# Kernel optimization log

Hardware: AMD Instinct MI355X
Metric: run time of the kernel (lower is better)

The kernel has to match this reference:

```python
import jax, jax.numpy as jnp
import numpy as np

B, S, H, K = 16, 1024, 1024, 256


def _span(x, Ws, bs, start, end):
    # x: [B,S,H]; start/end: [B,K] int indices into the S axis
    def proj(W, b):
        return jnp.einsum('bsh,oh->bso', x, W) + b  # nn.Linear: x @ W.T + b

    def gather(p, idx):
        # batched index_select along seq axis -> [B,K,H]
        return jnp.take_along_axis(p, idx[..., None], axis=1)

    p1, p2, p3, p4 = (proj(W, b) for W, b in zip(Ws, bs))
    span = (gather(p1, start) + gather(p2, end)
            + (gather(p3, start) - gather(p3, end))
            + gather(p4, start) * gather(p4, end))
    return jnp.tanh(span)


def setup_inputs() -> dict:
    key = jax.random.key(0)
    ks = jax.random.split(key, 20)
    inp = {
        'hidden_states': jax.random.normal(ks[0], (B, S, H), dtype=jnp.float32),
        'prem_word_idxs': jax.random.randint(ks[1], (B, 1, 2, K), 0, S, dtype=jnp.int64) if jax.config.read('jax_enable_x64') else jax.random.randint(ks[1], (B, 1, 2, K), 0, S).astype(jnp.int32),
        'hypo_word_idxs': jax.random.randint(ks[2], (B, 1, 2, K), 0, S).astype(jnp.int32),
    }
    names = ['Wp1', 'bp1', 'Wp2', 'bp2', 'Wp3', 'bp3', 'Wp4', 'bp4',
             'Wh1', 'bh1', 'Wh2', 'bh2', 'Wh3', 'bh3', 'Wh4', 'bh4']
    for i, n in enumerate(names):
        k = ks[3 + i]
        if n.startswith('W'):
            inp[n] = jax.random.normal(k, (H, H), dtype=jnp.float32) * 0.02
        else:
            inp[n] = jax.random.normal(k, (H,), dtype=jnp.float32) * 0.02
    return inp


def reference(hidden_states, prem_word_idxs, hypo_word_idxs,
              Wp1, bp1, Wp2, bp2, Wp3, bp3, Wp4, bp4,
              Wh1, bh1, Wh2, bh2, Wh3, bh3, Wh4, bh4):
    p_idx = prem_word_idxs[:, 0]  # squeeze(1) -> [B,2,K]
    h_idx = hypo_word_idxs[:, 0]
    prem_h_ij = _span(hidden_states, (Wp1, Wp2, Wp3, Wp4), (bp1, bp2, bp3, bp4),
                      p_idx[:, 0], p_idx[:, 1])
    hypo_h_ij = _span(hidden_states, (Wh1, Wh2, Wh3, Wh4), (bh1, bh2, bh3, bh4),
                      h_idx[:, 0], h_idx[:, 1])
    return (prem_h_ij, hypo_h_ij)
```

## Files before the change

kernel.cpp:

```cpp
#include <hip/hip_runtime.h>
#include <hip/hip_bf16.h>

typedef _Float16 f16;
typedef _Float16 f16x4 __attribute__((ext_vector_type(4)));
typedef _Float16 f16x8 __attribute__((ext_vector_type(8)));
typedef float    f32x4 __attribute__((ext_vector_type(4)));

#define H_DIM 1024
#define S_DIM 1024
#define PLANE (1024*1024)
#define MT 128
#define NT 64
#define KT 32
#define XOFF (6*PLANE)

__device__ __forceinline__ void load_lds16(const f16* g, f16* l) {
    __builtin_amdgcn_global_load_lds(
        (const __attribute__((address_space(1))) void*)g,
        (__attribute__((address_space(3))) void*)l, 16, 0, 0);
}

__global__ __launch_bounds__(256) void prep_weights(
    const float* __restrict__ Wp1, const float* __restrict__ Wp2,
    const float* __restrict__ Wp3, const float* __restrict__ Wp4,
    const float* __restrict__ Wh1, const float* __restrict__ Wh2,
    const float* __restrict__ Wh3, const float* __restrict__ Wh4,
    f16* __restrict__ ws)
{
    const int span = blockIdx.y;
    const float* W1 = span ? Wh1 : Wp1;
    const float* W2 = span ? Wh2 : Wp2;
    const float* W3 = span ? Wh3 : Wp3;
    const float* W4 = span ? Wh4 : Wp4;
    f16* base = ws + (size_t)span * 3 * PLANE;

    size_t i = ((size_t)blockIdx.x * 256 + threadIdx.x) * 4;
    f32x4 w1 = *(const f32x4*)(W1 + i);
    f32x4 w2 = *(const f32x4*)(W2 + i);
    f32x4 w3 = *(const f32x4*)(W3 + i);
    f32x4 w4 = *(const f32x4*)(W4 + i);

    f16x4 wa, wb, wc;
#pragma unroll
    for (int j = 0; j < 4; ++j) {
        wa[j] = (f16)(w1[j] + w3[j]);
        wb[j] = (f16)(w2[j] - w3[j]);
        wc[j] = (f16)w4[j];
    }
    *(f16x4*)(base + 0*PLANE + i) = wa;
    *(f16x4*)(base + 1*PLANE + i) = wb;
    *(f16x4*)(base + 2*PLANE + i) = wc;
}

__global__ __launch_bounds__(256) void prep_x(const float* __restrict__ x,
                                              f16* __restrict__ xh)
{
    size_t i = ((size_t)blockIdx.x * 256 + threadIdx.x) * 4;
    f32x4 v = *(const f32x4*)(x + i);
    f16x4 h;
#pragma unroll
    for (int j = 0; j < 4; ++j) h[j] = (f16)v[j];
    *(f16x4*)(xh + i) = h;
}

__global__ __launch_bounds__(256) void span_gemm(
    const f16* __restrict__ xh,
    const int* __restrict__ idxP, const int* __restrict__ idxH,
    const f16* __restrict__ wpl,
    const float* __restrict__ bp1, const float* __restrict__ bp2, const float* __restrict__ bp4,
    const float* __restrict__ bh1, const float* __restrict__ bh2, const float* __restrict__ bh4,
    float* __restrict__ out)
{
    const int t     = threadIdx.x;
    const int mtile = blockIdx.x;
    const int ntile = blockIdx.y;
    const int span  = blockIdx.z;

    const int* idx   = span ? idxH : idxP;
    const f16* wbase = wpl + (size_t)span * 3 * PLANE;
    const float* b1 = span ? bh1 : bp1;
    const float* b2 = span ? bh2 : bp2;
    const float* b4 = span ? bh4 : bp4;
    float* obase = out + (size_t)span * 4096 * H_DIM;

    __shared__ __align__(16) f16 A_lds[2][2 * MT * KT];
    __shared__ __align__(16) f16 B_lds[2][3 * NT * KT];
    __shared__ int rowoff[2][MT];

    {
        int side = t >> 7;
        int m = t & 127;
        int bk = mtile * MT + m;
        int b  = bk >> 8;
        int kk = bk & 255;
        int id = idx[b * 512 + side * 256 + kk];
        rowoff[side][m] = (b * S_DIM + id) * H_DIM;
    }
    __syncthreads();

    const int wid  = t >> 6;
    const int lane = t & 63;

    const f16* asrc[4]; int adst[4];
#pragma unroll
    for (int j = 0; j < 4; ++j) {
        int o = wid * 4 + j;
        int p = o >> 3, g = o & 7;
        int r = g * 16 + (lane >> 2);
        asrc[j] = xh + rowoff[p][r] + (lane & 3) * 8;
        adst[j] = p * (MT * KT) + g * 16 * KT;
    }
    const f16* bsrc[3]; int bdst[3];
#pragma unroll
    for (int j = 0; j < 3; ++j) {
        int o = wid * 3 + j;
        int p = o >> 2, g = o & 3;
        int grow = ntile * NT + g * 16 + (lane >> 2);
        bsrc[j] = wbase + (size_t)p * PLANE + (size_t)grow * H_DIM + (lane & 3) * 8;
        bdst[j] = p * (NT * KT) + g * 16 * KT;
    }

    f32x4 accL[4][2], accP[4][2], accQ[4][2];
    {
        f32x4 z = {0.f, 0.f, 0.f, 0.f};
#pragma unroll
        for (int mf = 0; mf < 4; ++mf)
#pragma unroll
            for (int nf = 0; nf < 2; ++nf) { accL[mf][nf] = z; accP[mf][nf] = z; accQ[mf][nf] = z; }
    }

    const int wm   = (wid & 1) * 64;
    const int wn   = (wid >> 1) * 32;
    const int lrow = lane & 15;
    const int lq   = lane >> 4;

#pragma unroll
    for (int j = 0; j < 4; ++j) load_lds16(asrc[j], &A_lds[0][adst[j]]);
#pragma unroll
    for (int j = 0; j < 3; ++j) load_lds16(bsrc[j], &B_lds[0][bdst[j]]);
    __syncthreads();

    for (int ks = 0; ks < H_DIM / KT; ++ks) {
        const int cur = ks & 1;
        if (ks < H_DIM / KT - 1) {
            const int k0 = (ks + 1) * KT;
            const int nb = cur ^ 1;
#pragma unroll
            for (int j = 0; j < 4; ++j) load_lds16(asrc[j] + k0, &A_lds[nb][adst[j]]);
#pragma unroll
            for (int j = 0; j < 3; ++j) load_lds16(bsrc[j] + k0, &B_lds[nb][bdst[j]]);
        }

        f16x8 afr[2][4], bfr[3][2];
#pragma unroll
        for (int mf = 0; mf < 4; ++mf) {
            int r = (wm + mf * 16 + lrow) * KT + lq * 8;
            afr[0][mf] = *(const f16x8*)&A_lds[cur][r];
            afr[1][mf] = *(const f16x8*)&A_lds[cur][MT * KT + r];
        }
#pragma unroll
        for (int nf = 0; nf < 2; ++nf) {
            int r = (wn + nf * 16 + lrow) * KT + lq * 8;
#pragma unroll
            for (int p = 0; p < 3; ++p)
                bfr[p][nf] = *(const f16x8*)&B_lds[cur][p * (NT * KT) + r];
        }

#pragma unroll
        for (int mf = 0; mf < 4; ++mf)
#pragma unroll
            for (int nf = 0; nf < 2; ++nf) {
                accL[mf][nf] = __builtin_amdgcn_mfma_f32_16x16x32_f16(afr[0][mf], bfr[0][nf], accL[mf][nf], 0, 0, 0);
                accL[mf][nf] = __builtin_amdgcn_mfma_f32_16x16x32_f16(afr[1][mf], bfr[1][nf], accL[mf][nf], 0, 0, 0);
                accP[mf][nf] = __builtin_amdgcn_mfma_f32_16x16x32_f16(afr[0][mf], bfr[2][nf], accP[mf][nf], 0, 0, 0);
                accQ[mf][nf] = __builtin_amdgcn_mfma_f32_16x16x32_f16(afr[1][mf], bfr[2][nf], accQ[mf][nf], 0, 0, 0);
            }

        __syncthreads();
    }

#pragma unroll
    for (int mf = 0; mf < 4; ++mf)
#pragma unroll
        for (int nf = 0; nf < 2; ++nf) {
            int col = ntile * NT + wn + nf * 16 + lrow;
            float bb12 = b1[col] + b2[col];
            float bb4  = b4[col];
            int row0 = mtile * MT + wm + mf * 16 + lq * 4;
#pragma unroll
            for (int i = 0; i < 4; ++i) {
                float v = accL[mf][nf][i] + bb12
                        + (accP[mf][nf][i] + bb4) * (accQ[mf][nf][i] + bb4);
                obase[(size_t)(row0 + i) * H_DIM + col] = tanhf(v);
            }
        }
}

extern "C" void kernel_launch(void* const* d_in, const int* in_sizes, int n_in,
                              void* d_out, int out_size, void* d_ws, size_t ws_size,
                              hipStream_t stream) {
    (void)in_sizes; (void)n_in; (void)out_size; (void)ws_size;
    const float* x    = (const float*)d_in[0];
    const int*   idxP = (const int*)d_in[1];
    const int*   idxH = (const int*)d_in[2];
    const float* Wp1 = (const float*)d_in[3];  const float* bp1 = (const float*)d_in[4];
    const float* Wp2 = (const float*)d_in[5];  const float* bp2 = (const float*)d_in[6];
    const float* Wp3 = (const float*)d_in[7];
    const float* Wp4 = (const float*)d_in[9];  const float* bp4 = (const float*)d_in[10];
    const float* Wh1 = (const float*)d_in[11]; const float* bh1 = (const float*)d_in[12];
    const float* Wh2 = (const float*)d_in[13]; const float* bh2 = (const float*)d_in[14];
    const float* Wh3 = (const float*)d_in[15];
    const float* Wh4 = (const float*)d_in[17]; const float* bh4 = (const float*)d_in[18];
    float* out = (float*)d_out;
    f16*   ws  = (f16*)d_ws;

    prep_weights<<<dim3(1024, 2), 256, 0, stream>>>(Wp1, Wp2, Wp3, Wp4,
                                                    Wh1, Wh2, Wh3, Wh4, ws);
    prep_x<<<16384, 256, 0, stream>>>(x, ws + XOFF);
    span_gemm<<<dim3(32, 16, 2), 256, 0, stream>>>(ws + XOFF, idxP, idxH, ws,
                                                   bp1, bp2, bp4, bh1, bh2, bh4, out);
}
```

Measured before the change: 255.9 us.

## Load weight fragments directly to registers and deepen A-tile LDS pipeline

```diff
diff --git a/kernel.cpp b/kernel.cpp
--- a/kernel.cpp
+++ b/kernel.cpp
@@ -12,6 +12,8 @@
 #define MT 128
 #define NT 64
 #define KT 32
+#define AP (MT*KT)
+#define ABUF (2*AP)
 #define XOFF (6*PLANE)
 
 __device__ __forceinline__ void load_lds16(const f16* g, f16* l) {
@@ -63,6 +65,40 @@
     *(f16x4*)(xh + i) = h;
 }
 
+#define K_STEP(ks_, BU, BF)                                                    \
+  {                                                                            \
+    const int kv = (ks_);                                                      \
+    if (kv < 31) {                                                             \
+      _Pragma("unroll")                                                        \
+      for (int j = 0; j < 6; ++j) { BF[j] = *(const f16x8*)bp[j]; bp[j] += KT; } \
+    }                                                                          \
+    if (kv < 31) __asm__ volatile("s_waitcnt vmcnt(10)" ::: "memory");         \
+    else         __asm__ volatile("s_waitcnt vmcnt(0)"  ::: "memory");         \
+    __builtin_amdgcn_s_barrier();                                              \
+    if (kv < 30) {                                                             \
+      f16* dst = &A_all[((kv + 2) & 3) * ABUF];                                \
+      _Pragma("unroll")                                                        \
+      for (int j = 0; j < 4; ++j) { load_lds16(ap[j], dst + adst[j]); ap[j] += KT; } \
+    }                                                                          \
+    const f16* Ab = &A_all[(kv & 3) * ABUF];                                   \
+    f16x8 afr0[4], afr1[4];                                                    \
+    _Pragma("unroll")                                                          \
+    for (int mf = 0; mf < 4; ++mf) {                                           \
+      int r = (wm + mf * 16 + lrow) * KT + lq * 8;                             \
+      afr0[mf] = *(const f16x8*)&Ab[r];                                        \
+      afr1[mf] = *(const f16x8*)&Ab[AP + r];                                   \
+    }                                                                          \
+    _Pragma("unroll")                                                          \
+    for (int mf = 0; mf < 4; ++mf)                                             \
+      _Pragma("unroll")                                                        \
+      for (int nf = 0; nf < 2; ++nf) {                                         \
+        accL[mf][nf] = __builtin_amdgcn_mfma_f32_16x16x32_f16(afr0[mf], BU[0*2+nf], accL[mf][nf], 0,0,0); \
+        accL[mf][nf] = __builtin_amdgcn_mfma_f32_16x16x32_f16(afr1[mf], BU[1*2+nf], accL[mf][nf], 0,0,0); \
+        accP[mf][nf] = __builtin_amdgcn_mfma_f32_16x16x32_f16(afr0[mf], BU[2*2+nf], accP[mf][nf], 0,0,0); \
+        accQ[mf][nf] = __builtin_amdgcn_mfma_f32_16x16x32_f16(afr1[mf], BU[2*2+nf], accQ[mf][nf], 0,0,0); \
+      }                                                                        \
+  }
+
 __global__ __launch_bounds__(256) void span_gemm(
     const f16* __restrict__ xh,
     const int* __restrict__ idxP, const int* __restrict__ idxH,
@@ -83,41 +119,41 @@
     const float* b4 = span ? bh4 : bp4;
     float* obase = out + (size_t)span * 4096 * H_DIM;
 
-    __shared__ __align__(16) f16 A_lds[2][2 * MT * KT];
-    __shared__ __align__(16) f16 B_lds[2][3 * NT * KT];
-    __shared__ int rowoff[2][MT];
-
+    __shared__ __align__(16) f16 A_all[4 * ABUF];
+
+    int* rowoff = (int*)A_all;
     {
-        int side = t >> 7;
-        int m = t & 127;
+        int side = t >> 7, m = t & 127;
         int bk = mtile * MT + m;
-        int b  = bk >> 8;
-        int kk = bk & 255;
-        int id = idx[b * 512 + side * 256 + kk];
-        rowoff[side][m] = (b * S_DIM + id) * H_DIM;
+        int b  = bk >> 8, kk = bk & 255;
+        rowoff[side * 128 + m] = (b * S_DIM + idx[b * 512 + side * 256 + kk]) * H_DIM;
     }
     __syncthreads();
 
     const int wid  = t >> 6;
     const int lane = t & 63;
-
-    const f16* asrc[4]; int adst[4];
+    const int wm   = (wid & 1) * 64;
+    const int wn   = (wid >> 1) * 32;
+    const int lrow = lane & 15;
+    const int lq   = lane >> 4;
+
+    const f16* ap[4]; int adst[4];
 #pragma unroll
     for (int j = 0; j < 4; ++j) {
         int o = wid * 4 + j;
         int p = o >> 3, g = o & 7;
         int r = g * 16 + (lane >> 2);
-        asrc[j] = xh + rowoff[p][r] + (lane & 3) * 8;
-        adst[j] = p * (MT * KT) + g * 16 * KT;
-    }
-    const f16* bsrc[3]; int bdst[3];
-#pragma unroll
-    for (int j = 0; j < 3; ++j) {
-        int o = wid * 3 + j;
-        int p = o >> 2, g = o & 3;
-        int grow = ntile * NT + g * 16 + (lane >> 2);
-        bsrc[j] = wbase + (size_t)p * PLANE + (size_t)grow * H_DIM + (lane & 3) * 8;
-        bdst[j] = p * (NT * KT) + g * 16 * KT;
+        ap[j]   = xh + rowoff[p * 128 + r] + (lane & 3) * 8;
+        adst[j] = p * AP + g * 16 * KT;
+    }
+    __syncthreads();
+
+    const f16* bp[6];
+#pragma unroll
+    for (int j = 0; j < 6; ++j) {
+        int p = j >> 1, nf = j & 1;
+        int row = ntile * NT + wn + nf * 16 + lrow;
+        bp[j] = wbase + (size_t)p * PLANE + (size_t)row * H_DIM + lq * 8;
     }
 
     f32x4 accL[4][2], accP[4][2], accQ[4][2];
@@ -129,54 +165,17 @@
             for (int nf = 0; nf < 2; ++nf) { accL[mf][nf] = z; accP[mf][nf] = z; accQ[mf][nf] = z; }
     }
 
-    const int wm   = (wid & 1) * 64;
-    const int wn   = (wid >> 1) * 32;
-    const int lrow = lane & 15;
-    const int lq   = lane >> 4;
-
-#pragma unroll
-    for (int j = 0; j < 4; ++j) load_lds16(asrc[j], &A_lds[0][adst[j]]);
-#pragma unroll
-    for (int j = 0; j < 3; ++j) load_lds16(bsrc[j], &B_lds[0][bdst[j]]);
-    __syncthreads();
-
-    for (int ks = 0; ks < H_DIM / KT; ++ks) {
-        const int cur = ks & 1;
-        if (ks < H_DIM / KT - 1) {
-            const int k0 = (ks + 1) * KT;
-            const int nb = cur ^ 1;
-#pragma unroll
-            for (int j = 0; j < 4; ++j) load_lds16(asrc[j] + k0, &A_lds[nb][adst[j]]);
-#pragma unroll
-            for (int j = 0; j < 3; ++j) load_lds16(bsrc[j] + k0, &B_lds[nb][bdst[j]]);
-        }
-
-        f16x8 afr[2][4], bfr[3][2];
-#pragma unroll
-        for (int mf = 0; mf < 4; ++mf) {
-            int r = (wm + mf * 16 + lrow) * KT + lq * 8;
-            afr[0][mf] = *(const f16x8*)&A_lds[cur][r];
-            afr[1][mf] = *(const f16x8*)&A_lds[cur][MT * KT + r];
-        }
-#pragma unroll
-        for (int nf = 0; nf < 2; ++nf) {
-            int r = (wn + nf * 16 + lrow) * KT + lq * 8;
-#pragma unroll
-            for (int p = 0; p < 3; ++p)
-                bfr[p][nf] = *(const f16x8*)&B_lds[cur][p * (NT * KT) + r];
-        }
-
-#pragma unroll
-        for (int mf = 0; mf < 4; ++mf)
-#pragma unroll
-            for (int nf = 0; nf < 2; ++nf) {
-                accL[mf][nf] = __builtin_amdgcn_mfma_f32_16x16x32_f16(afr[0][mf], bfr[0][nf], accL[mf][nf], 0, 0, 0);
-                accL[mf][nf] = __builtin_amdgcn_mfma_f32_16x16x32_f16(afr[1][mf], bfr[1][nf], accL[mf][nf], 0, 0, 0);
-                accP[mf][nf] = __builtin_amdgcn_mfma_f32_16x16x32_f16(afr[0][mf], bfr[2][nf], accP[mf][nf], 0, 0, 0);
-                accQ[mf][nf] = __builtin_amdgcn_mfma_f32_16x16x32_f16(afr[1][mf], bfr[2][nf], accQ[mf][nf], 0, 0, 0);
-            }
-
-        __syncthreads();
+    f16x8 bfr0[6], bfr1[6];
+#pragma unroll
+    for (int j = 0; j < 4; ++j) { load_lds16(ap[j], &A_all[0 * ABUF + adst[j]]); ap[j] += KT; }
+#pragma unroll
+    for (int j = 0; j < 6; ++j) { bfr0[j] = *(const f16x8*)bp[j]; bp[j] += KT; }
+#pragma unroll
+    for (int j = 0; j < 4; ++j) { load_lds16(ap[j], &A_all[1 * ABUF + adst[j]]); ap[j] += KT; }
+
+    for (int ks = 0; ks < 32; ks += 2) {
+        K_STEP(ks,     bfr0, bfr1);
+        K_STEP(ks + 1, bfr1, bfr0);
     }
 
 #pragma unroll
```

Result: slower. 322.3 us (+25.9%).
